# Kernel optimization log

Measured on AMD Instinct MI355X. Metric: run time of the kernel, lower is better.

Reference implementation:

```python
import jax, jax.numpy as jnp
import numpy as np
from jax import lax

EPS = 1e-12  # F.normalize eps
NEG_MAX = float(np.finfo(np.float32).max)


def _l2norm(x, axis):
    n = jnp.sqrt(jnp.sum(x * x, axis=axis, keepdims=True))
    return x / jnp.maximum(n, EPS)


def setup_inputs() -> dict:
    key = jax.random.key(0)
    k1, k2, k3 = jax.random.split(key, 3)
    B, T, C, E = 32, 2048, 2048, 64
    hidden_states = jax.random.normal(k1, (B, T, C), dtype=jnp.float32)
    sim_matrix = jax.random.normal(k2, (C, E), dtype=jnp.float32)
    gates = jax.random.normal(k3, (E,), dtype=jnp.float32)
    return {"hidden_states": hidden_states, "sim_matrix": sim_matrix, "gates": gates}


def reference(hidden_states, sim_matrix, gates):
    B, T, C = hidden_states.shape
    E = gates.shape[0]
    # mean over sequence -> [B, C]
    seq_rep = jnp.mean(hidden_states, axis=1)
    # cosine-similarity gating: normalize rows of seq_rep, columns of sim_matrix
    token_affinity = jnp.matmul(_l2norm(seq_rep, axis=-1), _l2norm(sim_matrix, axis=0))  # [B, E]
    logits = token_affinity - jax.nn.sigmoid(gates)
    gated_logits = jax.nn.relu(logits)
    # STE forward: hard threshold
    activation_mask_seq = (gated_logits > 0).astype(gated_logits.dtype)  # [B, E]
    num_active = jnp.sum(activation_mask_seq, axis=1)
    inactive = num_active == 0  # [B]
    fallback_count = jnp.sum(inactive).astype(jnp.float32)
    # topk fallback for fully-inactive rows (computed for all rows, applied where inactive)
    k_fallback = E // 2
    _, fb_idx = lax.top_k(logits, k_fallback)  # [B, k]
    fb_mask = jnp.sum(jax.nn.one_hot(fb_idx, E, dtype=activation_mask_seq.dtype), axis=1)  # [B, E]
    activation_mask_seq = jnp.where(inactive[:, None], jnp.maximum(activation_mask_seq, fb_mask), activation_mask_seq)
    # masked softmax over experts
    gated_masked = jnp.where(activation_mask_seq > 0, gated_logits, -NEG_MAX)
    active_expert_probs_seq = jax.nn.softmax(gated_masked, axis=-1)  # [B, E]
    # expand over sequence
    active_expert_probs = jnp.broadcast_to(active_expert_probs_seq[:, None, :], (B, T, E))
    activation_mask = jnp.broadcast_to(activation_mask_seq[:, None, :], (B, T, E))
    return active_expert_probs, fallback_count, logits, activation_mask
```

## Files before the change

kernel.cpp:

```cpp
#include <hip/hip_runtime.h>
#include <math.h>

#define B_  32
#define T_  2048
#define C_  2048
#define E_  64
#define NT_ 8
#define TC_ (T_ / NT_)
#define C4_ (C_ / 4)

#define OFF_FB     (B_ * T_ * E_)
#define OFF_LOGITS (OFF_FB + 1)
#define OFF_MASK   (OFF_LOGITS + B_ * E_)

#define WS_PARTIAL 0
#define WS_FLAGS   (NT_ * B_ * C_)
#define WS_PROBS   (WS_FLAGS + B_)
#define WS_MASK    (WS_PROBS + B_ * E_)

__global__ __launch_bounds__(256) void k_partial(const float* __restrict__ hs,
                                                 float* __restrict__ partial) {
    int gid = blockIdx.x * 256 + threadIdx.x;
    int c4  = gid & (C4_ - 1);
    int r   = gid >> 9;
    int tc  = r & (NT_ - 1);
    int b   = r >> 3;

    const float4* hs4 = (const float4*)hs;
    long base = (long)(b * T_ + tc * TC_) * C4_ + c4;

    float4 a0 = make_float4(0.f, 0.f, 0.f, 0.f);
    float4 a1 = make_float4(0.f, 0.f, 0.f, 0.f);
    #pragma unroll 4
    for (int t = 0; t < TC_; t += 2) {
        float4 v0 = hs4[base + (long)t * C4_];
        float4 v1 = hs4[base + (long)(t + 1) * C4_];
        a0.x += v0.x; a0.y += v0.y; a0.z += v0.z; a0.w += v0.w;
        a1.x += v1.x; a1.y += v1.y; a1.z += v1.z; a1.w += v1.w;
    }
    float4 acc = make_float4(a0.x + a1.x, a0.y + a1.y, a0.z + a1.z, a0.w + a1.w);

    float4* p4 = (float4*)partial;
    p4[(tc * B_ + b) * C4_ + c4] = acc;
}

__global__ __launch_bounds__(256) void k_gate(const float* __restrict__ partial,
                                              const float* __restrict__ sim,
                                              const float* __restrict__ gates,
                                              float* __restrict__ out,
                                              float* __restrict__ ws_probs,
                                              float* __restrict__ ws_mask,
                                              float* __restrict__ ws_flags) {
    int b    = blockIdx.x;
    int tid  = threadIdx.x;
    int e    = tid & 63;
    int wseg = tid >> 6;

    __shared__ float red0[4][64];
    __shared__ float red1[4][64];
    __shared__ float red2[4][64];
    __shared__ float lds_logit[64];

    float dot = 0.f, wsq = 0.f, ssq = 0.f;
    const float invT = 1.0f / (float)T_;
    int c0 = wseg * (C_ / 4);
    for (int c = c0; c < c0 + C_ / 4; ++c) {
        float s = 0.f;
        #pragma unroll
        for (int tc = 0; tc < NT_; ++tc)
            s += partial[(tc * B_ + b) * C_ + c];
        s *= invT;
        float w = sim[c * E_ + e];
        dot = fmaf(s, w, dot);
        wsq = fmaf(w, w, wsq);
        ssq = fmaf(s, s, ssq);
    }
    red0[wseg][e] = dot;
    red1[wseg][e] = wsq;
    red2[wseg][e] = ssq;
    __syncthreads();

    float logit = 0.f;
    bool  active = false;
    if (tid < 64) {
        dot = red0[0][e] + red0[1][e] + red0[2][e] + red0[3][e];
        wsq = red1[0][e] + red1[1][e] + red1[2][e] + red1[3][e];
        ssq = red2[0][e] + red2[1][e] + red2[2][e] + red2[3][e];
        float ns  = fmaxf(sqrtf(ssq), 1e-12f);
        float nw  = fmaxf(sqrtf(wsq), 1e-12f);
        float aff = dot / (ns * nw);
        float g   = gates[e];
        float sig = 1.0f / (1.0f + expf(-g));
        logit  = aff - sig;
        active = (logit > 0.0f);
        lds_logit[e] = logit;
    }
    __syncthreads();

    if (tid < 64) {
        unsigned long long bal = __ballot(active);
        bool inactive = (bal == 0ULL);

        int rank = 0;
        for (int j = 0; j < 64; ++j) {
            float lj = lds_logit[j];
            rank += (int)((lj > logit) || (lj == logit && j < e));
        }
        bool fb = (rank < (E_ / 2));
        bool m  = inactive ? fb : active;

        float gated = fmaxf(logit, 0.0f);
        float me = m ? gated : -3.402823466e38f;

        float mx = me;
        #pragma unroll
        for (int off = 1; off < 64; off <<= 1)
            mx = fmaxf(mx, __shfl_xor(mx, off, 64));
        float p = expf(me - mx);
        float sum = p;
        #pragma unroll
        for (int off = 1; off < 64; off <<= 1)
            sum += __shfl_xor(sum, off, 64);
        float prob = p / sum;

        out[OFF_LOGITS + b * E_ + e] = logit;
        ws_probs[b * E_ + e] = prob;
        ws_mask[b * E_ + e]  = m ? 1.0f : 0.0f;
        if (e == 0) ws_flags[b] = inactive ? 1.0f : 0.0f;
    }
}

__global__ __launch_bounds__(256) void k_bcast(const float* __restrict__ ws_probs,
                                               const float* __restrict__ ws_mask,
                                               const float* __restrict__ ws_flags,
                                               float* __restrict__ out) {
    int gid = blockIdx.x * 256 + threadIdx.x;
    int e   = gid & (E_ - 1);
    int bt  = gid >> 6;
    int b   = bt >> 11;
    float p = ws_probs[b * E_ + e];
    float m = ws_mask[b * E_ + e];
    out[gid] = p;
    out[OFF_MASK + gid] = m;
    if (gid == 0) {
        float fc = 0.f;
        for (int i = 0; i < B_; ++i) fc += ws_flags[i];
        out[OFF_FB] = fc;
    }
}

extern "C" void kernel_launch(void* const* d_in, const int* in_sizes, int n_in,
                              void* d_out, int out_size, void* d_ws, size_t ws_size,
                              hipStream_t stream) {
    const float* hs    = (const float*)d_in[0];
    const float* sim   = (const float*)d_in[1];
    const float* gates = (const float*)d_in[2];
    float* out = (float*)d_out;
    float* ws  = (float*)d_ws;

    float* partial = ws + WS_PARTIAL;
    float* flags   = ws + WS_FLAGS;
    float* probs   = ws + WS_PROBS;
    float* maskv   = ws + WS_MASK;

    hipLaunchKernelGGL(k_partial, dim3(B_ * NT_ * C4_ / 256), dim3(256), 0, stream,
                       hs, partial);
    hipLaunchKernelGGL(k_gate, dim3(B_), dim3(256), 0, stream,
                       partial, sim, gates, out, probs, maskv, flags);
    hipLaunchKernelGGL(k_bcast, dim3(B_ * T_ * E_ / 256), dim3(256), 0, stream,
                       probs, maskv, flags, out);
}
```

Baseline: 793.5 us.

## Vectorize broadcast stores, split sequence finer, stage mean in LDS for gating

Splits the sequence reduction into 16 chunks instead of 8 so more blocks run in parallel, and unrolls the accumulation over 4 independent float4 accumulators. The gate kernel now reduces the partial sums once with float4 loads into shared memory, instead of re-reading them per expert thread. The broadcast kernel writes float4 stores, and handles the misaligned mask region with an offset-by-3 vector store plus scalar edge writes. This cuts redundant global reads in the gate kernel and the number of store instructions in the large broadcast, at the cost of more complex indexing.

```diff
diff --git a/kernel.cpp b/kernel.cpp
--- a/kernel.cpp
+++ b/kernel.cpp
@@ -5,13 +5,15 @@
 #define T_  2048
 #define C_  2048
 #define E_  64
-#define NT_ 8
+#define NT_ 16
 #define TC_ (T_ / NT_)
 #define C4_ (C_ / 4)
 
 #define OFF_FB     (B_ * T_ * E_)
 #define OFF_LOGITS (OFF_FB + 1)
 #define OFF_MASK   (OFF_LOGITS + B_ * E_)
+#define NBT_       (B_ * T_ * E_)
+#define NQ_        (NBT_ / 4)
 
 #define WS_PARTIAL 0
 #define WS_FLAGS   (NT_ * B_ * C_)
@@ -24,24 +26,28 @@
     int c4  = gid & (C4_ - 1);
     int r   = gid >> 9;
     int tc  = r & (NT_ - 1);
-    int b   = r >> 3;
+    int b   = r >> 4;
 
     const float4* hs4 = (const float4*)hs;
-    long base = (long)(b * T_ + tc * TC_) * C4_ + c4;
+    int base = (b * T_ + tc * TC_) * C4_ + c4;
 
     float4 a0 = make_float4(0.f, 0.f, 0.f, 0.f);
-    float4 a1 = make_float4(0.f, 0.f, 0.f, 0.f);
-    #pragma unroll 4
-    for (int t = 0; t < TC_; t += 2) {
-        float4 v0 = hs4[base + (long)t * C4_];
-        float4 v1 = hs4[base + (long)(t + 1) * C4_];
+    float4 a1 = a0, a2 = a0, a3 = a0;
+    for (int t = 0; t < TC_; t += 4) {
+        float4 v0 = hs4[base + (t + 0) * C4_];
+        float4 v1 = hs4[base + (t + 1) * C4_];
+        float4 v2 = hs4[base + (t + 2) * C4_];
+        float4 v3 = hs4[base + (t + 3) * C4_];
         a0.x += v0.x; a0.y += v0.y; a0.z += v0.z; a0.w += v0.w;
         a1.x += v1.x; a1.y += v1.y; a1.z += v1.z; a1.w += v1.w;
-    }
-    float4 acc = make_float4(a0.x + a1.x, a0.y + a1.y, a0.z + a1.z, a0.w + a1.w);
-
-    float4* p4 = (float4*)partial;
-    p4[(tc * B_ + b) * C4_ + c4] = acc;
+        a2.x += v2.x; a2.y += v2.y; a2.z += v2.z; a2.w += v2.w;
+        a3.x += v3.x; a3.y += v3.y; a3.z += v3.z; a3.w += v3.w;
+    }
+    float4 acc = make_float4(a0.x + a1.x + a2.x + a3.x,
+                             a0.y + a1.y + a2.y + a3.y,
+                             a0.z + a1.z + a2.z + a3.z,
+                             a0.w + a1.w + a2.w + a3.w);
+    ((float4*)partial)[(tc * B_ + b) * C4_ + c4] = acc;
 }
 
 __global__ __launch_bounds__(256) void k_gate(const float* __restrict__ partial,
@@ -51,44 +57,64 @@
                                               float* __restrict__ ws_probs,
                                               float* __restrict__ ws_mask,
                                               float* __restrict__ ws_flags) {
-    int b    = blockIdx.x;
-    int tid  = threadIdx.x;
-    int e    = tid & 63;
-    int wseg = tid >> 6;
-
-    __shared__ float red0[4][64];
-    __shared__ float red1[4][64];
-    __shared__ float red2[4][64];
+    int b   = blockIdx.x;
+    int tid = threadIdx.x;
+    int e   = tid & 63;
+    int w   = tid >> 6;
+
+    __shared__ float s_sh[C_];
+    __shared__ float redd[4][64];
+    __shared__ float redw[4][64];
+    __shared__ float red_ssq[4];
     __shared__ float lds_logit[64];
 
-    float dot = 0.f, wsq = 0.f, ssq = 0.f;
+    const float4* p4 = (const float4*)partial;
+    float4 m0 = make_float4(0.f, 0.f, 0.f, 0.f);
+    float4 m1 = m0;
+    #pragma unroll
+    for (int tc = 0; tc < NT_; ++tc) {
+        int o = (tc * B_ + b) * C4_;
+        float4 v0 = p4[o + tid];
+        float4 v1 = p4[o + tid + 256];
+        m0.x += v0.x; m0.y += v0.y; m0.z += v0.z; m0.w += v0.w;
+        m1.x += v1.x; m1.y += v1.y; m1.z += v1.z; m1.w += v1.w;
+    }
     const float invT = 1.0f / (float)T_;
-    int c0 = wseg * (C_ / 4);
+    m0.x *= invT; m0.y *= invT; m0.z *= invT; m0.w *= invT;
+    m1.x *= invT; m1.y *= invT; m1.z *= invT; m1.w *= invT;
+    ((float4*)s_sh)[tid]       = m0;
+    ((float4*)s_sh)[tid + 256] = m1;
+
+    float ssq = m0.x * m0.x + m0.y * m0.y + m0.z * m0.z + m0.w * m0.w
+              + m1.x * m1.x + m1.y * m1.y + m1.z * m1.z + m1.w * m1.w;
+    #pragma unroll
+    for (int off = 1; off < 64; off <<= 1)
+        ssq += __shfl_xor(ssq, off, 64);
+    if (e == 0) red_ssq[w] = ssq;
+    __syncthreads();
+    float ssq_tot = red_ssq[0] + red_ssq[1] + red_ssq[2] + red_ssq[3];
+
+    float dot = 0.f, wsq = 0.f;
+    int c0 = w * (C_ / 4);
+    #pragma unroll 4
     for (int c = c0; c < c0 + C_ / 4; ++c) {
-        float s = 0.f;
-        #pragma unroll
-        for (int tc = 0; tc < NT_; ++tc)
-            s += partial[(tc * B_ + b) * C_ + c];
-        s *= invT;
-        float w = sim[c * E_ + e];
-        dot = fmaf(s, w, dot);
-        wsq = fmaf(w, w, wsq);
-        ssq = fmaf(s, s, ssq);
-    }
-    red0[wseg][e] = dot;
-    red1[wseg][e] = wsq;
-    red2[wseg][e] = ssq;
+        float wv = sim[c * E_ + e];
+        float sv = s_sh[c];
+        dot = fmaf(sv, wv, dot);
+        wsq = fmaf(wv, wv, wsq);
+    }
+    redd[w][e] = dot;
+    redw[w][e] = wsq;
     __syncthreads();
 
     float logit = 0.f;
     bool  active = false;
     if (tid < 64) {
-        dot = red0[0][e] + red0[1][e] + red0[2][e] + red0[3][e];
-        wsq = red1[0][e] + red1[1][e] + red1[2][e] + red1[3][e];
-        ssq = red2[0][e] + red2[1][e] + red2[2][e] + red2[3][e];
-        float ns  = fmaxf(sqrtf(ssq), 1e-12f);
-        float nw  = fmaxf(sqrtf(wsq), 1e-12f);
-        float aff = dot / (ns * nw);
+        float d = redd[0][e] + redd[1][e] + redd[2][e] + redd[3][e];
+        float q = redw[0][e] + redw[1][e] + redw[2][e] + redw[3][e];
+        float ns  = fmaxf(sqrtf(ssq_tot), 1e-12f);
+        float nw  = fmaxf(sqrtf(q), 1e-12f);
+        float aff = d / (ns * nw);
         float g   = gates[e];
         float sig = 1.0f / (1.0f + expf(-g));
         logit  = aff - sig;
@@ -102,6 +128,7 @@
         bool inactive = (bal == 0ULL);
 
         int rank = 0;
+        #pragma unroll
         for (int j = 0; j < 64; ++j) {
             float lj = lds_logit[j];
             rank += (int)((lj > logit) || (lj == logit && j < e));
@@ -134,17 +161,27 @@
                                                const float* __restrict__ ws_mask,
                                                const float* __restrict__ ws_flags,
                                                float* __restrict__ out) {
-    int gid = blockIdx.x * 256 + threadIdx.x;
-    int e   = gid & (E_ - 1);
-    int bt  = gid >> 6;
-    int b   = bt >> 11;
-    float p = ws_probs[b * E_ + e];
-    float m = ws_mask[b * E_ + e];
-    out[gid] = p;
-    out[OFF_MASK + gid] = m;
-    if (gid == 0) {
+    int i = blockIdx.x * 256 + threadIdx.x;
+    int b = i >> 15;
+    ((float4*)out)[i] = ((const float4*)ws_probs)[(b << 4) | (i & 15)];
+
+    if (i < NQ_ - 1) {
+        int f = 3 + 4 * i;
+        float4 mv;
+        mv.x = ws_mask[(((f + 0) >> 17) << 6) | ((f + 0) & 63)];
+        mv.y = ws_mask[(((f + 1) >> 17) << 6) | ((f + 1) & 63)];
+        mv.z = ws_mask[(((f + 2) >> 17) << 6) | ((f + 2) & 63)];
+        mv.w = ws_mask[(((f + 3) >> 17) << 6) | ((f + 3) & 63)];
+        ((float4*)(out + OFF_MASK + 3))[i] = mv;
+    }
+    if (i == 0) {
+        out[OFF_MASK + 0] = ws_mask[0];
+        out[OFF_MASK + 1] = ws_mask[1];
+        out[OFF_MASK + 2] = ws_mask[2];
+        out[OFF_MASK + NBT_ - 1] = ws_mask[B_ * E_ - 1];
         float fc = 0.f;
-        for (int i = 0; i < B_; ++i) fc += ws_flags[i];
+        #pragma unroll
+        for (int k = 0; k < B_; ++k) fc += ws_flags[k];
         out[OFF_FB] = fc;
     }
 }
@@ -167,6 +204,6 @@
                        hs, partial);
     hipLaunchKernelGGL(k_gate, dim3(B_), dim3(256), 0, stream,
                        partial, sim, gates, out, probs, maskv, flags);
-    hipLaunchKernelGGL(k_bcast, dim3(B_ * T_ * E_ / 256), dim3(256), 0, stream,
+    hipLaunchKernelGGL(k_bcast, dim3(NQ_ / 256), dim3(256), 0, stream,
                        probs, maskv, flags, out);
 }
```

Result: faster. 739.6 us (-6.8%).
